# Kernel tuning notes

Hardware: AMD Instinct MI355X
Metric: run time of the kernel (lower is better)

The kernel has to match this reference:

```python
import jax, jax.numpy as jnp
import numpy as np

N, K, CIN, HID, COUT, E, MH = 8192, 200, 512, 256, 40, 5, 64
KG = K // E
EPS = 1e-5


def setup_inputs() -> dict:
    key = jax.random.key(0)
    ks = jax.random.split(key, 20)
    inp = {
        "X": jax.random.normal(ks[0], (N, CIN), jnp.float32),
        "La": jax.random.uniform(ks[1], (K,), jnp.float32),
        "U": jax.random.normal(ks[2], (N, K), jnp.float32),
        # 5 EigenExperts, each mlp = Linear(1,64) -> ReLU -> Linear(64,64) -> ReLU -> Linear(64,1)
        "eW1": jax.random.normal(ks[3], (E, MH), jnp.float32) * 0.5,
        "eb1": jax.random.normal(ks[4], (E, MH), jnp.float32) * 0.1,
        "eW2": jax.random.normal(ks[5], (E, MH, MH), jnp.float32) * (1.0 / np.sqrt(MH)),
        "eb2": jax.random.normal(ks[6], (E, MH), jnp.float32) * 0.1,
        "eW3": jax.random.normal(ks[7], (E, MH), jnp.float32) * (1.0 / np.sqrt(MH)),
        "eb3": jax.random.normal(ks[8], (E,), jnp.float32) * 0.1,
        # gate: Linear(5,5) -> ReLU -> Linear(5,5) -> Softmax
        "gW1": jax.random.normal(ks[9], (E, E), jnp.float32) * 0.4,
        "gb1": jax.random.normal(ks[10], (E,), jnp.float32) * 0.1,
        "gW2": jax.random.normal(ks[11], (E, E), jnp.float32) * 0.4,
        "gb2": jax.random.normal(ks[12], (E,), jnp.float32) * 0.1,
        # W: Linear(in_channels, hidden_dim)
        "Ww": jax.random.normal(ks[13], (CIN, HID), jnp.float32) * (1.0 / np.sqrt(CIN)),
        "Wb": jax.random.normal(ks[14], (HID,), jnp.float32) * 0.1,
        # BatchNorm1d(hidden_dim), training-mode batch stats
        "bn_gamma": jnp.ones((HID,), jnp.float32),
        "bn_beta": jnp.zeros((HID,), jnp.float32),
        # MLP: Linear(hidden_dim, out_channels)
        "Mw": jax.random.normal(ks[15], (HID, COUT), jnp.float32) * (1.0 / np.sqrt(HID)),
        "Mb": jax.random.normal(ks[16], (COUT,), jnp.float32) * 0.1,
    }
    return inp


def reference(X, La, U, eW1, eb1, eW2, eb2, eW3, eb3, gW1, gb1, gW2, gb2, Ww, Wb, bn_gamma, bn_beta, Mw, Mb):
    n, k = U.shape
    e = eW1.shape[0]
    kg = k // e
    # group eigenvector columns: U[:, i*kg:(i+1)*kg] for expert i -> [n, e, kg]
    Ue = U.reshape(n, e, kg)
    # EigenExpert tiny MLP applied elementwise over entries of each column, then mean over nodes
    h1 = jax.nn.relu(jnp.einsum('nek,eh->nekh', Ue, eW1) + eb1[None, :, None, :])
    h2 = jax.nn.relu(jnp.einsum('nekh,ehg->nekg', h1, eW2) + eb2[None, :, None, :])
    v = jnp.einsum('nekh,eh->nek', h2, eW3) + eb3[None, :, None]
    V = v.mean(axis=0)                      # [e, kg] importance per eigenvector
    # gate on per-group mean eigenvalue
    stats = La.reshape(e, kg).mean(axis=1)  # [e]
    g = jax.nn.relu(stats @ gW1 + gb1) @ gW2 + gb2
    g = jax.nn.softmax(g, axis=-1)          # [e]
    # sum_i g_i * U_i diag(V_i) U_i^T == (U * s) @ U^T with per-column scale s
    s = (g[:, None] * V).reshape(k)         # [k]
    A = (U * s[None, :]) @ U.T              # [n, n]
    out = A @ X                             # [n, cin]
    hidden = out @ Ww + Wb                  # [n, hid]
    mu = hidden.mean(axis=0)
    var = hidden.var(axis=0)                # biased, as torch BN uses for normalization
    h = (hidden - mu) * jax.lax.rsqrt(var + EPS) * bn_gamma + bn_beta
    h = jax.nn.relu(h)                      # dropout is identity (eval)
    logits = h @ Mw + Mb
    return jax.nn.log_softmax(logits, axis=1), hidden
```

## Files before the change

### kernel.cpp

```cpp
#include <hip/hip_runtime.h>
#include <hip/hip_bf16.h>

#define N_    8192
#define K_    200
#define CIN_  512
#define HID_  256
#define COUT_ 40
#define E_    5
#define MH_   64
#define KG_   40
#define EPS_  1e-5f

#define WS_VSUM  0
#define WS_BNSUM 256
#define WS_T     768
#define WS_S     103168
#define WS_G     103424

typedef __bf16 bf16x8 __attribute__((ext_vector_type(8)));
typedef _Float16 f16x2 __attribute__((ext_vector_type(2)));
typedef _Float16 f16x8 __attribute__((ext_vector_type(8)));
typedef float  f32x16 __attribute__((ext_vector_type(16)));

__device__ __forceinline__ uint packbf(float a, float b) {
    union { __bf16 h[2]; uint u; } p;
    p.h[0] = (__bf16)a; p.h[1] = (__bf16)b;
    return p.u;
}

union UB { uint4 q; bf16x8 v; };
union UHF { f16x2 h2[4]; f16x8 v; };

__global__ __launch_bounds__(256) void k_expert(
    const float* __restrict__ U,
    const float* __restrict__ eW1, const float* __restrict__ eb1,
    const float* __restrict__ eW2, const float* __restrict__ eb2,
    const float* __restrict__ eW3, const float* __restrict__ eb3,
    float* __restrict__ Vsum)
{
    const int e   = blockIdx.x;
    const int tid = threadIdx.x;
    const int w   = tid >> 6;
    const int l   = tid & 63;
    const int lo  = l & 31;
    const int hi  = l >> 5;

    __shared__ f16x2 sW1h[32], sb1h[32];
    __shared__ float sb2s[MH_], sW3s[MH_];
    __shared__ float colsum[4][48];

    if (tid < 32) {
        f16x2 w2; w2.x = (_Float16)eW1[e*MH_ + 2*tid]; w2.y = (_Float16)eW1[e*MH_ + 2*tid + 1];
        sW1h[tid] = w2;
        f16x2 b2; b2.x = (_Float16)eb1[e*MH_ + 2*tid]; b2.y = (_Float16)eb1[e*MH_ + 2*tid + 1];
        sb1h[tid] = b2;
    }
    if (tid < MH_) {
        sb2s[tid] = eb2[e*MH_ + tid];
        sW3s[tid] = eW3[e*MH_ + tid];
    }
    if (tid < 192) colsum[tid / 48][tid % 48] = 0.f;
    const float b3 = eb3[e];

    UHF fa[2][4];
    {
        const float* W2e = eW2 + e*MH_*MH_;
        #pragma unroll
        for (int mt = 0; mt < 2; ++mt) {
            const int grow = mt*32 + lo;
            #pragma unroll
            for (int t = 0; t < 4; ++t) {
                const int k0 = 16*t + 8*hi;
                #pragma unroll
                for (int r = 0; r < 4; ++r) {
                    f16x2 p;
                    p.x = (_Float16)W2e[(k0+2*r  )*MH_ + grow];
                    p.y = (_Float16)W2e[(k0+2*r+1)*MH_ + grow];
                    fa[mt][t].h2[r] = p;
                }
            }
        }
    }
    __syncthreads();

    f32x16 ci0, ci1;
    #pragma unroll
    for (int r = 0; r < 16; ++r) {
        const int gb = (r & 3) + 8*(r >> 2) + 4*hi;
        ci0[r] = sb2s[gb];
        ci1[r] = sb2s[32 + gb];
    }

    float uu[4]; int kgs[4];
    const int tile0 = blockIdx.y*16 + w*4;
    #pragma unroll
    for (int it = 0; it < 4; ++it) {
        const int idx = (tile0 + it)*32 + lo;
        const int n   = idx / KG_;
        const int kg  = idx - n*KG_;
        uu[it]  = U[n*K_ + e*KG_ + kg];
        kgs[it] = kg;
    }

    const f16x2 z2 = {(_Float16)0.f, (_Float16)0.f};

    #pragma unroll
    for (int it = 0; it < 4; ++it) {
        f16x2 u2; u2.x = (_Float16)uu[it]; u2.y = u2.x;

        f32x16 a0, a1;
        #pragma unroll
        for (int t = 0; t < 4; ++t) {
            const int kp = 8*t + 4*hi;
            UHF b;
            #pragma unroll
            for (int r = 0; r < 4; ++r)
                b.h2[r] = __builtin_elementwise_max(u2*sW1h[kp + r] + sb1h[kp + r], z2);
            if (t == 0) {
                a0 = __builtin_amdgcn_mfma_f32_32x32x16_f16(fa[0][0].v, b.v, ci0, 0, 0, 0);
                a1 = __builtin_amdgcn_mfma_f32_32x32x16_f16(fa[1][0].v, b.v, ci1, 0, 0, 0);
            } else {
                a0 = __builtin_amdgcn_mfma_f32_32x32x16_f16(fa[0][t].v, b.v, a0, 0, 0, 0);
                a1 = __builtin_amdgcn_mfma_f32_32x32x16_f16(fa[1][t].v, b.v, a1, 0, 0, 0);
            }
        }

        float p0 = 0.f, p1 = 0.f, p2 = 0.f, p3 = 0.f;
        #pragma unroll
        for (int r = 0; r < 16; r += 2) {
            const int g0 = (r & 3) + 8*(r >> 2) + 4*hi;
            const int g1 = ((r+1) & 3) + 8*((r+1) >> 2) + 4*hi;
            p0 += fmaxf(a0[r],   0.f) * sW3s[g0];
            p1 += fmaxf(a1[r],   0.f) * sW3s[32 + g0];
            p2 += fmaxf(a0[r+1], 0.f) * sW3s[g1];
            p3 += fmaxf(a1[r+1], 0.f) * sW3s[32 + g1];
        }
        float vs = (p0 + p1) + (p2 + p3);
        vs += __shfl_xor(vs, 32);
        if (hi == 0) atomicAdd(&colsum[w][kgs[it]], vs + b3);
    }

    __syncthreads();
    if (tid < KG_)
        atomicAdd(&Vsum[e*KG_ + tid],
                  colsum[0][tid] + colsum[1][tid] + colsum[2][tid] + colsum[3][tid]);
}

__global__ void k_gate(
    const float* __restrict__ La,
    const float* __restrict__ gW1, const float* __restrict__ gb1,
    const float* __restrict__ gW2, const float* __restrict__ gb2,
    const float* __restrict__ Vsum, float* __restrict__ s)
{
    __shared__ float sg[E_];
    const int tid = threadIdx.x;
    if (tid == 0) {
        float stats[E_], g1[E_], g2[E_];
        for (int e = 0; e < E_; ++e) {
            float acc = 0.f;
            for (int k = 0; k < KG_; ++k) acc += La[e*KG_ + k];
            stats[e] = acc * (1.0f/KG_);
        }
        for (int j = 0; j < E_; ++j) {
            float acc = gb1[j];
            for (int i = 0; i < E_; ++i) acc += stats[i]*gW1[i*E_ + j];
            g1[j] = fmaxf(acc, 0.f);
        }
        float m = -1e30f;
        for (int j = 0; j < E_; ++j) {
            float acc = gb2[j];
            for (int i = 0; i < E_; ++i) acc += g1[i]*gW2[i*E_ + j];
            g2[j] = acc;
            m = fmaxf(m, acc);
        }
        float ssum = 0.f;
        for (int j = 0; j < E_; ++j) { g2[j] = expf(g2[j]-m); ssum += g2[j]; }
        for (int j = 0; j < E_; ++j) sg[j] = g2[j] / ssum;
    }
    __syncthreads();
    if (tid < K_) s[tid] = sg[tid / KG_] * Vsum[tid] * (1.0f/N_);
}

__global__ __launch_bounds__(256) void k_utx(
    const float* __restrict__ U, const float* __restrict__ X,
    float* __restrict__ P)
{
    const int nc0 = blockIdx.x * 64;
    const int mc0 = blockIdx.y * 64;
    const int ks  = blockIdx.z;
    const int r0  = ks * 512;
    const int tid = threadIdx.x;
    const int w   = tid >> 6, l = tid & 63, lo = l & 31, hi = l >> 5;
    const int mq  = w >> 1, nq = w & 1;

    __shared__ uint sU[2][32][68];
    __shared__ uint sX[2][32][68];

    const int rpA = tid >> 4;
    const int rpB = rpA + 16;
    const int c4  = tid & 15;
    const int mcA = mc0 + 4*c4;
    const int xcA = nc0 + 4*c4;
    const int UMAX = N_*K_ - 4;

    float4 uA0,uA1,uB0,uB1,xA0,xA1,xB0,xB1;

#define UTX_LD(chunk) {                                                       \
    const int rb_ = r0 + 64*(chunk);                                          \
    uA0 = *reinterpret_cast<const float4*>(&U[min((rb_+2*rpA  )*K_ + mcA, UMAX)]); \
    uA1 = *reinterpret_cast<const float4*>(&U[min((rb_+2*rpA+1)*K_ + mcA, UMAX)]); \
    uB0 = *reinterpret_cast<const float4*>(&U[min((rb_+2*rpB  )*K_ + mcA, UMAX)]); \
    uB1 = *reinterpret_cast<const float4*>(&U[min((rb_+2*rpB+1)*K_ + mcA, UMAX)]); \
    xA0 = *reinterpret_cast<const float4*>(&X[(rb_+2*rpA  )*CIN_ + xcA]);     \
    xA1 = *reinterpret_cast<const float4*>(&X[(rb_+2*rpA+1)*CIN_ + xcA]);     \
    xB0 = *reinterpret_cast<const float4*>(&X[(rb_+2*rpB  )*CIN_ + xcA]);     \
    xB1 = *reinterpret_cast<const float4*>(&X[(rb_+2*rpB+1)*CIN_ + xcA]); }

#define UTX_WR(buf) {                                                         \
    uint4 p_;                                                                 \
    p_.x = packbf(uA0.x,uA1.x); p_.y = packbf(uA0.y,uA1.y);                   \
    p_.z = packbf(uA0.z,uA1.z); p_.w = packbf(uA0.w,uA1.w);                   \
    *reinterpret_cast<uint4*>(&sU[buf][rpA][4*c4]) = p_;                      \
    p_.x = packbf(uB0.x,uB1.x); p_.y = packbf(uB0.y,uB1.y);                   \
    p_.z = packbf(uB0.z,uB1.z); p_.w = packbf(uB0.w,uB1.w);                   \
    *reinterpret_cast<uint4*>(&sU[buf][rpB][4*c4]) = p_;                      \
    p_.x = packbf(xA0.x,xA1.x); p_.y = packbf(xA0.y,xA1.y);                   \
    p_.z = packbf(xA0.z,xA1.z); p_.w = packbf(xA0.w,xA1.w);                   \
    *reinterpret_cast<uint4*>(&sX[buf][rpA][4*c4]) = p_;                      \
    p_.x = packbf(xB0.x,xB1.x); p_.y = packbf(xB0.y,xB1.y);                   \
    p_.z = packbf(xB0.z,xB1.z); p_.w = packbf(xB0.w,xB1.w);                   \
    *reinterpret_cast<uint4*>(&sX[buf][rpB][4*c4]) = p_; }

#define UTX_MM(buf) {                                                         \
    _Pragma("unroll") for (int ksi = 0; ksi < 4; ++ksi) {                     \
        const int rp0_ = 8*ksi + 4*hi;                                        \
        UB a_, b_;                                                            \
        a_.q.x = sU[buf][rp0_+0][32*mq+lo];                                   \
        a_.q.y = sU[buf][rp0_+1][32*mq+lo];                                   \
        a_.q.z = sU[buf][rp0_+2][32*mq+lo];                                   \
        a_.q.w = sU[buf][rp0_+3][32*mq+lo];                                   \
        b_.q.x = sX[buf][rp0_+0][32*nq+lo];                                   \
        b_.q.y = sX[buf][rp0_+1][32*nq+lo];                                   \
        b_.q.z = sX[buf][rp0_+2][32*nq+lo];                                   \
        b_.q.w = sX[buf][rp0_+3][32*nq+lo];                                   \
        acc = __builtin_amdgcn_mfma_f32_32x32x16_bf16(a_.v, b_.v, acc, 0,0,0); } }

    f32x16 acc = {0};
    UTX_LD(0);
    UTX_WR(0);
    __syncthreads();
    #pragma unroll
    for (int t = 0; t < 8; ++t) {
        if (t < 7) UTX_LD(t+1);
        UTX_MM(t & 1);
        if (t < 7) UTX_WR((t+1) & 1);
        __syncthreads();
    }

    #pragma unroll
    for (int r = 0; r < 16; ++r) {
        const int mrow = mc0 + mq*32 + (r & 3) + 8*(r >> 2) + 4*hi;
        const int ncol = nc0 + nq*32 + lo;
        P[(ks*256 + mrow)*512 + ncol] = acc[r];
    }
#undef UTX_LD
#undef UTX_WR
#undef UTX_MM
}

__global__ __launch_bounds__(256) void k_red(
    const float* __restrict__ P, float* __restrict__ T)
{
    const int j  = blockIdx.x*256 + threadIdx.x;
    const int m  = j >> 7;
    const int c4 = j & 127;
    float4 s4 = {0.f, 0.f, 0.f, 0.f};
    for (int ks = 0; ks < 16; ++ks) {
        const float4 v = *reinterpret_cast<const float4*>(&P[(ks*256 + m)*512 + 4*c4]);
        s4.x += v.x; s4.y += v.y; s4.z += v.z; s4.w += v.w;
    }
    *reinterpret_cast<float4*>(&T[m*512 + 4*c4]) = s4;
}

__global__ __launch_bounds__(256) void k_g(
    const float* __restrict__ T, const float* __restrict__ Ww,
    float* __restrict__ G)
{
    const int k0  = blockIdx.x * 4;
    const int c   = threadIdx.x;
    __shared__ float4 sT4[4][128];

    for (int j = threadIdx.x; j < 512; j += 256) {
        const int r = j >> 7, c4 = j & 127;
        sT4[r][c4] = reinterpret_cast<const float4*>(T)[(k0+r)*128 + c4];
    }
    __syncthreads();

    float a0 = 0.f, a1 = 0.f, a2 = 0.f, a3 = 0.f;
    for (int ci4 = 0; ci4 < 128; ++ci4) {
        const float w0 = Ww[(4*ci4+0)*HID_ + c];
        const float w1 = Ww[(4*ci4+1)*HID_ + c];
        const float w2 = Ww[(4*ci4+2)*HID_ + c];
        const float w3 = Ww[(4*ci4+3)*HID_ + c];
        float4 t;
        t = sT4[0][ci4]; a0 += t.x*w0 + t.y*w1 + t.z*w2 + t.w*w3;
        t = sT4[1][ci4]; a1 += t.x*w0 + t.y*w1 + t.z*w2 + t.w*w3;
        t = sT4[2][ci4]; a2 += t.x*w0 + t.y*w1 + t.z*w2 + t.w*w3;
        t = sT4[3][ci4]; a3 += t.x*w0 + t.y*w1 + t.z*w2 + t.w*w3;
    }
    G[(k0+0)*HID_ + c] = a0;
    G[(k0+1)*HID_ + c] = a1;
    G[(k0+2)*HID_ + c] = a2;
    G[(k0+3)*HID_ + c] = a3;
}

__global__ __launch_bounds__(256) void k_hidden(
    const float* __restrict__ U, const float* __restrict__ s,
    const float* __restrict__ G, const float* __restrict__ Wb,
    float* __restrict__ hid, float* __restrict__ bnsum)
{
    const int c0  = blockIdx.x * 32;
    const int n0  = blockIdx.y * 128;
    const int tid = threadIdx.x;
    const int w   = tid >> 6;
    const int l   = tid & 63;
    const int lo  = l & 31;
    const int hi  = l >> 5;

    __shared__ uint  sA[104][129];
    __shared__ uint  sB[104][33];
    __shared__ float ss[208];

    if (tid < 208) ss[tid] = (tid < K_) ? s[tid] : 0.f;
    __syncthreads();

    #pragma unroll
    for (int u = 0; u < 13; ++u) {
        const int j  = tid + u*256;
        const int m  = j & 127, kq = j >> 7;
        float4 a = {0,0,0,0}, b = {0,0,0,0};
        if (kq < 25) {
            a = *reinterpret_cast<const float4*>(&U[(n0+m)*K_ + 8*kq]);
            b = *reinterpret_cast<const float4*>(&U[(n0+m)*K_ + 8*kq + 4]);
            a.x *= ss[8*kq+0]; a.y *= ss[8*kq+1]; a.z *= ss[8*kq+2]; a.w *= ss[8*kq+3];
            b.x *= ss[8*kq+4]; b.y *= ss[8*kq+5]; b.z *= ss[8*kq+6]; b.w *= ss[8*kq+7];
        }
        sA[4*kq+0][m] = packbf(a.x, a.y);
        sA[4*kq+1][m] = packbf(a.z, a.w);
        sA[4*kq+2][m] = packbf(b.x, b.y);
        sA[4*kq+3][m] = packbf(b.z, b.w);
    }
    for (int j = tid; j < 832; j += 256) {
        const int c = j & 31, kq = j >> 5;
        float g[8];
        #pragma unroll
        for (int i = 0; i < 8; ++i)
            g[i] = (kq < 25) ? G[(8*kq+i)*HID_ + c0 + c] : 0.f;
        sB[4*kq+0][c] = packbf(g[0], g[1]);
        sB[4*kq+1][c] = packbf(g[2], g[3]);
        sB[4*kq+2][c] = packbf(g[4], g[5]);
        sB[4*kq+3][c] = packbf(g[6], g[7]);
    }
    __syncthreads();

    f32x16 acc = {0};
    #pragma unroll
    for (int t = 0; t < 13; ++t) {
        const int rp0 = 8*t + 4*hi;
        UB a_, b_;
        a_.q.x = sA[rp0+0][32*w + lo];
        a_.q.y = sA[rp0+1][32*w + lo];
        a_.q.z = sA[rp0+2][32*w + lo];
        a_.q.w = sA[rp0+3][32*w + lo];
        b_.q.x = sB[rp0+0][lo];
        b_.q.y = sB[rp0+1][lo];
        b_.q.z = sB[rp0+2][lo];
        b_.q.w = sB[rp0+3][lo];
        acc = __builtin_amdgcn_mfma_f32_32x32x16_bf16(a_.v, b_.v, acc, 0, 0, 0);
    }

    const float wb = Wb[c0 + lo];
    float sm = 0.f, sq = 0.f;
    #pragma unroll
    for (int r = 0; r < 16; ++r) {
        const int row = 32*w + (r & 3) + 8*(r >> 2) + 4*hi;
        const float h = acc[r] + wb;
        hid[(n0+row)*HID_ + c0 + lo] = h;
        sm += h; sq += h*h;
    }
    sm += __shfl_xor(sm, 32); sq += __shfl_xor(sq, 32);
    if (hi == 0) {
        atomicAdd(&bnsum[c0 + lo],        sm);
        atomicAdd(&bnsum[HID_ + c0 + lo], sq);
    }
}

__global__ __launch_bounds__(256) void k_logits(
    const float* __restrict__ hid, const float* __restrict__ bnsum,
    const float* __restrict__ gamma, const float* __restrict__ beta,
    const float* __restrict__ Mw, const float* __restrict__ Mb,
    float* __restrict__ outls)
{
    __shared__ float sc[HID_], sh[HID_], sMb[COUT_];
    __shared__ float sMw[HID_][COUT_];
    __shared__ float sPart[8][32][41];

    const int tid = threadIdx.x;
    const int r   = tid & 31;
    const int sl  = tid >> 5;

    {
        const float sm = bnsum[tid], sq = bnsum[HID_+tid];
        const float mu  = sm * (1.0f/N_);
        const float var = sq * (1.0f/N_) - mu*mu;
        const float a   = gamma[tid] * rsqrtf(var + EPS_);
        sc[tid] = a;
        sh[tid] = beta[tid] - mu*a;
    }
    for (int j = tid; j < HID_*COUT_/4; j += 256)
        reinterpret_cast<float4*>(&sMw[0][0])[j] = reinterpret_cast<const float4*>(Mw)[j];
    if (tid < COUT_) sMb[tid] = Mb[tid];
    __syncthreads();

    const int n  = blockIdx.x*32 + r;
    const int cb = sl * 32;
    float acc[COUT_];
    #pragma unroll
    for (int j = 0; j < COUT_; ++j) acc[j] = 0.f;

    const float4* hrow = reinterpret_cast<const float4*>(&hid[n*HID_ + cb]);
    #pragma unroll
    for (int c4 = 0; c4 < 8; ++c4) {
        const float4 h4 = hrow[c4];
        const float hv[4] = {h4.x, h4.y, h4.z, h4.w};
        #pragma unroll
        for (int q = 0; q < 4; ++q) {
            const int c = cb + 4*c4 + q;
            const float hn = fmaxf(hv[q]*sc[c] + sh[c], 0.f);
            #pragma unroll
            for (int j0 = 0; j0 < COUT_; j0 += 4) {
                const float4 wv = *reinterpret_cast<const float4*>(&sMw[c][j0]);
                acc[j0+0] += hn*wv.x; acc[j0+1] += hn*wv.y;
                acc[j0+2] += hn*wv.z; acc[j0+3] += hn*wv.w;
            }
        }
    }
    #pragma unroll
    for (int j = 0; j < COUT_; ++j) sPart[sl][r][j] = acc[j];
    __syncthreads();

    if (tid < 32) {
        const int n2 = blockIdx.x*32 + tid;
        float a2[COUT_];
        #pragma unroll
        for (int j = 0; j < COUT_; ++j) {
            float sum = sMb[j];
            #pragma unroll
            for (int s2 = 0; s2 < 8; ++s2) sum += sPart[s2][tid][j];
            a2[j] = sum;
        }
        float m = -1e30f;
        #pragma unroll
        for (int j = 0; j < COUT_; ++j) m = fmaxf(m, a2[j]);
        float ssum = 0.f;
        #pragma unroll
        for (int j = 0; j < COUT_; ++j) ssum += expf(a2[j] - m);
        const float lse = m + logf(ssum);
        #pragma unroll
        for (int j = 0; j < COUT_; ++j)
            outls[n2*COUT_ + j] = a2[j] - lse;
    }
}

extern "C" void kernel_launch(void* const* d_in, const int* in_sizes, int n_in,
                              void* d_out, int out_size, void* d_ws, size_t ws_size,
                              hipStream_t stream)
{
    const float* X        = (const float*)d_in[0];
    const float* La       = (const float*)d_in[1];
    const float* U        = (const float*)d_in[2];
    const float* eW1      = (const float*)d_in[3];
    const float* eb1      = (const float*)d_in[4];
    const float* eW2      = (const float*)d_in[5];
    const float* eb2      = (const float*)d_in[6];
    const float* eW3      = (const float*)d_in[7];
    const float* eb3      = (const float*)d_in[8];
    const float* gW1      = (const float*)d_in[9];
    const float* gb1      = (const float*)d_in[10];
    const float* gW2      = (const float*)d_in[11];
    const float* gb2      = (const float*)d_in[12];
    const float* Ww       = (const float*)d_in[13];
    const float* Wb       = (const float*)d_in[14];
    const float* bn_gamma = (const float*)d_in[15];
    const float* bn_beta  = (const float*)d_in[16];
    const float* Mw       = (const float*)d_in[17];
    const float* Mb       = (const float*)d_in[18];

    float* out   = (float*)d_out;
    float* ws    = (float*)d_ws;
    float* Vsum  = ws + WS_VSUM;
    float* bnsum = ws + WS_BNSUM;
    float* T     = ws + WS_T;
    float* s     = ws + WS_S;
    float* G     = ws + WS_G;

    float* outls = out;
    float* hid   = out + N_*COUT_;
    float* P     = out;

    (void)hipMemsetAsync(ws, 0, (size_t)768 * sizeof(float), stream);

    k_utx   <<<dim3(8, 4, 16), 256, 0, stream>>>(U, X, P);
    k_expert<<<dim3(E_, 640),  256, 0, stream>>>(U, eW1, eb1, eW2, eb2, eW3, eb3, Vsum);
    k_gate  <<<1,   256, 0, stream>>>(La, gW1, gb1, gW2, gb2, Vsum, s);
    k_red   <<<100, 256, 0, stream>>>(P, T);
    k_g     <<<50,  256, 0, stream>>>(T, Ww, G);
    k_hidden<<<dim3(8, 64), 256, 0, stream>>>(U, s, G, Wb, hid, bnsum);
    k_logits<<<256, 256, 0, stream>>>(hid, bnsum, bn_gamma, bn_beta, Mw, Mb, outls);
}
```

Baseline: 210.7 us.

## Merge U^T X and expert kernels into one launch; fuse reduce, gate and G

```diff
diff --git a/kernel.cpp b/kernel.cpp
--- a/kernel.cpp
+++ b/kernel.cpp
@@ -13,7 +13,6 @@
 
 #define WS_VSUM  0
 #define WS_BNSUM 256
-#define WS_T     768
 #define WS_S     103168
 #define WS_G     103424
 
@@ -31,179 +30,41 @@
 union UB { uint4 q; bf16x8 v; };
 union UHF { f16x2 h2[4]; f16x8 v; };
 
-__global__ __launch_bounds__(256) void k_expert(
-    const float* __restrict__ U,
+__global__ __launch_bounds__(256) void k_fused1(
+    const float* __restrict__ U, const float* __restrict__ X,
+    float* __restrict__ P,
     const float* __restrict__ eW1, const float* __restrict__ eb1,
     const float* __restrict__ eW2, const float* __restrict__ eb2,
     const float* __restrict__ eW3, const float* __restrict__ eb3,
     float* __restrict__ Vsum)
 {
-    const int e   = blockIdx.x;
+    __shared__ __align__(16) char ldsraw[34816];
     const int tid = threadIdx.x;
     const int w   = tid >> 6;
     const int l   = tid & 63;
     const int lo  = l & 31;
     const int hi  = l >> 5;
 
-    __shared__ f16x2 sW1h[32], sb1h[32];
-    __shared__ float sb2s[MH_], sW3s[MH_];
-    __shared__ float colsum[4][48];
-
-    if (tid < 32) {
-        f16x2 w2; w2.x = (_Float16)eW1[e*MH_ + 2*tid]; w2.y = (_Float16)eW1[e*MH_ + 2*tid + 1];
-        sW1h[tid] = w2;
-        f16x2 b2; b2.x = (_Float16)eb1[e*MH_ + 2*tid]; b2.y = (_Float16)eb1[e*MH_ + 2*tid + 1];
-        sb1h[tid] = b2;
-    }
-    if (tid < MH_) {
-        sb2s[tid] = eb2[e*MH_ + tid];
-        sW3s[tid] = eW3[e*MH_ + tid];
-    }
-    if (tid < 192) colsum[tid / 48][tid % 48] = 0.f;
-    const float b3 = eb3[e];
-
-    UHF fa[2][4];
-    {
-        const float* W2e = eW2 + e*MH_*MH_;
-        #pragma unroll
-        for (int mt = 0; mt < 2; ++mt) {
-            const int grow = mt*32 + lo;
-            #pragma unroll
-            for (int t = 0; t < 4; ++t) {
-                const int k0 = 16*t + 8*hi;
-                #pragma unroll
-                for (int r = 0; r < 4; ++r) {
-                    f16x2 p;
-                    p.x = (_Float16)W2e[(k0+2*r  )*MH_ + grow];
-                    p.y = (_Float16)W2e[(k0+2*r+1)*MH_ + grow];
-                    fa[mt][t].h2[r] = p;
-                }
-            }
-        }
-    }
-    __syncthreads();
-
-    f32x16 ci0, ci1;
-    #pragma unroll
-    for (int r = 0; r < 16; ++r) {
-        const int gb = (r & 3) + 8*(r >> 2) + 4*hi;
-        ci0[r] = sb2s[gb];
-        ci1[r] = sb2s[32 + gb];
-    }
-
-    float uu[4]; int kgs[4];
-    const int tile0 = blockIdx.y*16 + w*4;
-    #pragma unroll
-    for (int it = 0; it < 4; ++it) {
-        const int idx = (tile0 + it)*32 + lo;
-        const int n   = idx / KG_;
-        const int kg  = idx - n*KG_;
-        uu[it]  = U[n*K_ + e*KG_ + kg];
-        kgs[it] = kg;
-    }
-
-    const f16x2 z2 = {(_Float16)0.f, (_Float16)0.f};
-
-    #pragma unroll
-    for (int it = 0; it < 4; ++it) {
-        f16x2 u2; u2.x = (_Float16)uu[it]; u2.y = u2.x;
-
-        f32x16 a0, a1;
-        #pragma unroll
-        for (int t = 0; t < 4; ++t) {
-            const int kp = 8*t + 4*hi;
-            UHF b;
-            #pragma unroll
-            for (int r = 0; r < 4; ++r)
-                b.h2[r] = __builtin_elementwise_max(u2*sW1h[kp + r] + sb1h[kp + r], z2);
-            if (t == 0) {
-                a0 = __builtin_amdgcn_mfma_f32_32x32x16_f16(fa[0][0].v, b.v, ci0, 0, 0, 0);
-                a1 = __builtin_amdgcn_mfma_f32_32x32x16_f16(fa[1][0].v, b.v, ci1, 0, 0, 0);
-            } else {
-                a0 = __builtin_amdgcn_mfma_f32_32x32x16_f16(fa[0][t].v, b.v, a0, 0, 0, 0);
-                a1 = __builtin_amdgcn_mfma_f32_32x32x16_f16(fa[1][t].v, b.v, a1, 0, 0, 0);
-            }
-        }
-
-        float p0 = 0.f, p1 = 0.f, p2 = 0.f, p3 = 0.f;
-        #pragma unroll
-        for (int r = 0; r < 16; r += 2) {
-            const int g0 = (r & 3) + 8*(r >> 2) + 4*hi;
-            const int g1 = ((r+1) & 3) + 8*((r+1) >> 2) + 4*hi;
-            p0 += fmaxf(a0[r],   0.f) * sW3s[g0];
-            p1 += fmaxf(a1[r],   0.f) * sW3s[32 + g0];
-            p2 += fmaxf(a0[r+1], 0.f) * sW3s[g1];
-            p3 += fmaxf(a1[r+1], 0.f) * sW3s[32 + g1];
-        }
-        float vs = (p0 + p1) + (p2 + p3);
-        vs += __shfl_xor(vs, 32);
-        if (hi == 0) atomicAdd(&colsum[w][kgs[it]], vs + b3);
-    }
-
-    __syncthreads();
-    if (tid < KG_)
-        atomicAdd(&Vsum[e*KG_ + tid],
-                  colsum[0][tid] + colsum[1][tid] + colsum[2][tid] + colsum[3][tid]);
-}
-
-__global__ void k_gate(
-    const float* __restrict__ La,
-    const float* __restrict__ gW1, const float* __restrict__ gb1,
-    const float* __restrict__ gW2, const float* __restrict__ gb2,
-    const float* __restrict__ Vsum, float* __restrict__ s)
-{
-    __shared__ float sg[E_];
-    const int tid = threadIdx.x;
-    if (tid == 0) {
-        float stats[E_], g1[E_], g2[E_];
-        for (int e = 0; e < E_; ++e) {
-            float acc = 0.f;
-            for (int k = 0; k < KG_; ++k) acc += La[e*KG_ + k];
-            stats[e] = acc * (1.0f/KG_);
-        }
-        for (int j = 0; j < E_; ++j) {
-            float acc = gb1[j];
-            for (int i = 0; i < E_; ++i) acc += stats[i]*gW1[i*E_ + j];
-            g1[j] = fmaxf(acc, 0.f);
-        }
-        float m = -1e30f;
-        for (int j = 0; j < E_; ++j) {
-            float acc = gb2[j];
-            for (int i = 0; i < E_; ++i) acc += g1[i]*gW2[i*E_ + j];
-            g2[j] = acc;
-            m = fmaxf(m, acc);
-        }
-        float ssum = 0.f;
-        for (int j = 0; j < E_; ++j) { g2[j] = expf(g2[j]-m); ssum += g2[j]; }
-        for (int j = 0; j < E_; ++j) sg[j] = g2[j] / ssum;
-    }
-    __syncthreads();
-    if (tid < K_) s[tid] = sg[tid / KG_] * Vsum[tid] * (1.0f/N_);
-}
-
-__global__ __launch_bounds__(256) void k_utx(
-    const float* __restrict__ U, const float* __restrict__ X,
-    float* __restrict__ P)
-{
-    const int nc0 = blockIdx.x * 64;
-    const int mc0 = blockIdx.y * 64;
-    const int ks  = blockIdx.z;
-    const int r0  = ks * 512;
-    const int tid = threadIdx.x;
-    const int w   = tid >> 6, l = tid & 63, lo = l & 31, hi = l >> 5;
-    const int mq  = w >> 1, nq = w & 1;
-
-    __shared__ uint sU[2][32][68];
-    __shared__ uint sX[2][32][68];
-
-    const int rpA = tid >> 4;
-    const int rpB = rpA + 16;
-    const int c4  = tid & 15;
-    const int mcA = mc0 + 4*c4;
-    const int xcA = nc0 + 4*c4;
-    const int UMAX = N_*K_ - 4;
-
-    float4 uA0,uA1,uB0,uB1,xA0,xA1,xB0,xB1;
+    if (blockIdx.x < 512) {
+        const int bid = blockIdx.x;
+        const int nc0 = (bid & 7) * 64;
+        const int mc0 = ((bid >> 3) & 3) * 64;
+        const int ks  = bid >> 5;
+        const int r0  = ks * 512;
+        const int mq  = w >> 1, nq = w & 1;
+
+        typedef uint UtxBuf[32][68];
+        UtxBuf* sU = reinterpret_cast<UtxBuf*>(ldsraw);
+        UtxBuf* sX = reinterpret_cast<UtxBuf*>(ldsraw + 17408);
+
+        const int rpA = tid >> 4;
+        const int rpB = rpA + 16;
+        const int c4  = tid & 15;
+        const int mcA = mc0 + 4*c4;
+        const int xcA = nc0 + 4*c4;
+        const int UMAX = N_*K_ - 4;
+
+        float4 uA0,uA1,uB0,uB1,xA0,xA1,xB0,xB1;
 
 #define UTX_LD(chunk) {                                                       \
     const int rb_ = r0 + 64*(chunk);                                          \
@@ -245,57 +106,195 @@
         b_.q.w = sX[buf][rp0_+3][32*nq+lo];                                   \
         acc = __builtin_amdgcn_mfma_f32_32x32x16_bf16(a_.v, b_.v, acc, 0,0,0); } }
 
-    f32x16 acc = {0};
-    UTX_LD(0);
-    UTX_WR(0);
-    __syncthreads();
-    #pragma unroll
-    for (int t = 0; t < 8; ++t) {
-        if (t < 7) UTX_LD(t+1);
-        UTX_MM(t & 1);
-        if (t < 7) UTX_WR((t+1) & 1);
+        f32x16 acc = {0};
+        UTX_LD(0);
+        UTX_WR(0);
         __syncthreads();
-    }
-
-    #pragma unroll
-    for (int r = 0; r < 16; ++r) {
-        const int mrow = mc0 + mq*32 + (r & 3) + 8*(r >> 2) + 4*hi;
-        const int ncol = nc0 + nq*32 + lo;
-        P[(ks*256 + mrow)*512 + ncol] = acc[r];
-    }
+        #pragma unroll
+        for (int t = 0; t < 8; ++t) {
+            if (t < 7) UTX_LD(t+1);
+            UTX_MM(t & 1);
+            if (t < 7) UTX_WR((t+1) & 1);
+            __syncthreads();
+        }
+
+        #pragma unroll
+        for (int r = 0; r < 16; ++r) {
+            const int mrow = mc0 + mq*32 + (r & 3) + 8*(r >> 2) + 4*hi;
+            const int ncol = nc0 + nq*32 + lo;
+            P[(ks*256 + mrow)*512 + ncol] = acc[r];
+        }
 #undef UTX_LD
 #undef UTX_WR
 #undef UTX_MM
+        return;
+    }
+
+    {
+        const int t5 = blockIdx.x - 512;
+        const int e  = t5 % E_;
+        const int by = t5 / E_;
+
+        struct ExLds {
+            f16x2 sW1h[32]; f16x2 sb1h[32];
+            float sb2s[MH_]; float sW3s[MH_];
+            float colsum[4][48];
+        };
+        ExLds& S = *reinterpret_cast<ExLds*>(ldsraw);
+
+        if (tid < 32) {
+            f16x2 w2; w2.x = (_Float16)eW1[e*MH_ + 2*tid]; w2.y = (_Float16)eW1[e*MH_ + 2*tid + 1];
+            S.sW1h[tid] = w2;
+            f16x2 b2; b2.x = (_Float16)eb1[e*MH_ + 2*tid]; b2.y = (_Float16)eb1[e*MH_ + 2*tid + 1];
+            S.sb1h[tid] = b2;
+        }
+        if (tid < MH_) {
+            S.sb2s[tid] = eb2[e*MH_ + tid];
+            S.sW3s[tid] = eW3[e*MH_ + tid];
+        }
+        if (tid < 192) S.colsum[tid / 48][tid % 48] = 0.f;
+        const float b3 = eb3[e];
+
+        UHF fa[2][4];
+        {
+            const float* W2e = eW2 + e*MH_*MH_;
+            #pragma unroll
+            for (int mt = 0; mt < 2; ++mt) {
+                const int grow = mt*32 + lo;
+                #pragma unroll
+                for (int t = 0; t < 4; ++t) {
+                    const int k0 = 16*t + 8*hi;
+                    #pragma unroll
+                    for (int r = 0; r < 4; ++r) {
+                        f16x2 p;
+                        p.x = (_Float16)W2e[(k0+2*r  )*MH_ + grow];
+                        p.y = (_Float16)W2e[(k0+2*r+1)*MH_ + grow];
+                        fa[mt][t].h2[r] = p;
+                    }
+                }
+            }
+        }
+        __syncthreads();
+
+        f32x16 ci0, ci1;
+        #pragma unroll
+        for (int r = 0; r < 16; ++r) {
+            const int gb = (r & 3) + 8*(r >> 2) + 4*hi;
+            ci0[r] = S.sb2s[gb];
+            ci1[r] = S.sb2s[32 + gb];
+        }
+
+        float uu[4]; int kgs[4];
+        const int tile0 = by*16 + w*4;
+        #pragma unroll
+        for (int it = 0; it < 4; ++it) {
+            const int idx = (tile0 + it)*32 + lo;
+            const int n   = idx / KG_;
+            const int kg  = idx - n*KG_;
+            uu[it]  = U[n*K_ + e*KG_ + kg];
+            kgs[it] = kg;
+        }
+
+        const f16x2 z2 = {(_Float16)0.f, (_Float16)0.f};
+
+        #pragma unroll
+        for (int it = 0; it < 4; ++it) {
+            f16x2 u2; u2.x = (_Float16)uu[it]; u2.y = u2.x;
+
+            f32x16 a0, a1;
+            #pragma unroll
+            for (int t = 0; t < 4; ++t) {
+                const int kp = 8*t + 4*hi;
+                UHF b;
+                #pragma unroll
+                for (int r = 0; r < 4; ++r)
+                    b.h2[r] = __builtin_elementwise_max(u2*S.sW1h[kp + r] + S.sb1h[kp + r], z2);
+                if (t == 0) {
+                    a0 = __builtin_amdgcn_mfma_f32_32x32x16_f16(fa[0][0].v, b.v, ci0, 0, 0, 0);
+                    a1 = __builtin_amdgcn_mfma_f32_32x32x16_f16(fa[1][0].v, b.v, ci1, 0, 0, 0);
+                } else {
+                    a0 = __builtin_amdgcn_mfma_f32_32x32x16_f16(fa[0][t].v, b.v, a0, 0, 0, 0);
+                    a1 = __builtin_amdgcn_mfma_f32_32x32x16_f16(fa[1][t].v, b.v, a1, 0, 0, 0);
+                }
+            }
+
+            float p0 = 0.f, p1 = 0.f, p2 = 0.f, p3 = 0.f;
+            #pragma unroll
+            for (int r = 0; r < 16; r += 2) {
+                const int g0 = (r & 3) + 8*(r >> 2) + 4*hi;
+                const int g1 = ((r+1) & 3) + 8*((r+1) >> 2) + 4*hi;
+                p0 += fmaxf(a0[r],   0.f) * S.sW3s[g0];
+                p1 += fmaxf(a1[r],   0.f) * S.sW3s[32 + g0];
+                p2 += fmaxf(a0[r+1], 0.f) * S.sW3s[g1];
+                p3 += fmaxf(a1[r+1], 0.f) * S.sW3s[32 + g1];
+            }
+            float vs = (p0 + p1) + (p2 + p3);
+            vs += __shfl_xor(vs, 32);
+            if (hi == 0) atomicAdd(&S.colsum[w][kgs[it]], vs + b3);
+        }
+
+        __syncthreads();
+        if (tid < KG_)
+            atomicAdd(&Vsum[e*KG_ + tid],
+                      S.colsum[0][tid] + S.colsum[1][tid] + S.colsum[2][tid] + S.colsum[3][tid]);
+    }
 }
 
-__global__ __launch_bounds__(256) void k_red(
-    const float* __restrict__ P, float* __restrict__ T)
+__global__ __launch_bounds__(256) void k_rgg(
+    const float* __restrict__ P, const float* __restrict__ Ww,
+    const float* __restrict__ La,
+    const float* __restrict__ gW1, const float* __restrict__ gb1,
+    const float* __restrict__ gW2, const float* __restrict__ gb2,
+    const float* __restrict__ Vsum,
+    float* __restrict__ s, float* __restrict__ G)
 {
-    const int j  = blockIdx.x*256 + threadIdx.x;
-    const int m  = j >> 7;
-    const int c4 = j & 127;
-    float4 s4 = {0.f, 0.f, 0.f, 0.f};
-    for (int ks = 0; ks < 16; ++ks) {
-        const float4 v = *reinterpret_cast<const float4*>(&P[(ks*256 + m)*512 + 4*c4]);
-        s4.x += v.x; s4.y += v.y; s4.z += v.z; s4.w += v.w;
-    }
-    *reinterpret_cast<float4*>(&T[m*512 + 4*c4]) = s4;
-}
-
-__global__ __launch_bounds__(256) void k_g(
-    const float* __restrict__ T, const float* __restrict__ Ww,
-    float* __restrict__ G)
-{
-    const int k0  = blockIdx.x * 4;
-    const int c   = threadIdx.x;
+    const int tid = threadIdx.x;
+
+    if (blockIdx.x == 50) {
+        __shared__ float sg[E_];
+        if (tid == 0) {
+            float stats[E_], g1[E_], g2[E_];
+            for (int e = 0; e < E_; ++e) {
+                float acc = 0.f;
+                for (int k = 0; k < KG_; ++k) acc += La[e*KG_ + k];
+                stats[e] = acc * (1.0f/KG_);
+            }
+            for (int j = 0; j < E_; ++j) {
+                float acc = gb1[j];
+                for (int i = 0; i < E_; ++i) acc += stats[i]*gW1[i*E_ + j];
+                g1[j] = fmaxf(acc, 0.f);
+            }
+            float m = -1e30f;
+            for (int j = 0; j < E_; ++j) {
+                float acc = gb2[j];
+                for (int i = 0; i < E_; ++i) acc += g1[i]*gW2[i*E_ + j];
+                g2[j] = acc;
+                m = fmaxf(m, acc);
+            }
+            float ssum = 0.f;
+            for (int j = 0; j < E_; ++j) { g2[j] = expf(g2[j]-m); ssum += g2[j]; }
+            for (int j = 0; j < E_; ++j) sg[j] = g2[j] / ssum;
+        }
+        __syncthreads();
+        if (tid < K_) s[tid] = sg[tid / KG_] * Vsum[tid] * (1.0f/N_);
+        return;
+    }
+
     __shared__ float4 sT4[4][128];
-
-    for (int j = threadIdx.x; j < 512; j += 256) {
+    const int k0 = blockIdx.x * 4;
+
+    for (int j = tid; j < 512; j += 256) {
         const int r = j >> 7, c4 = j & 127;
-        sT4[r][c4] = reinterpret_cast<const float4*>(T)[(k0+r)*128 + c4];
+        float4 a = {0.f, 0.f, 0.f, 0.f};
+        for (int ks = 0; ks < 16; ++ks) {
+            const float4 v = *reinterpret_cast<const float4*>(&P[(ks*256 + k0 + r)*512 + 4*c4]);
+            a.x += v.x; a.y += v.y; a.z += v.z; a.w += v.w;
+        }
+        sT4[r][c4] = a;
     }
     __syncthreads();
 
+    const int c = tid;
     float a0 = 0.f, a1 = 0.f, a2 = 0.f, a3 = 0.f;
     for (int ci4 = 0; ci4 < 128; ++ci4) {
         const float w0 = Ww[(4*ci4+0)*HID_ + c];
@@ -500,7 +499,6 @@
     float* ws    = (float*)d_ws;
     float* Vsum  = ws + WS_VSUM;
     float* bnsum = ws + WS_BNSUM;
-    float* T     = ws + WS_T;
     float* s     = ws + WS_S;
     float* G     = ws + WS_G;
 
@@ -510,11 +508,8 @@
 
     (void)hipMemsetAsync(ws, 0, (size_t)768 * sizeof(float), stream);
 
-    k_utx   <<<dim3(8, 4, 16), 256, 0, stream>>>(U, X, P);
-    k_expert<<<dim3(E_, 640),  256, 0, stream>>>(U, eW1, eb1, eW2, eb2, eW3, eb3, Vsum);
-    k_gate  <<<1,   256, 0, stream>>>(La, gW1, gb1, gW2, gb2, Vsum, s);
-    k_red   <<<100, 256, 0, stream>>>(P, T);
-    k_g     <<<50,  256, 0, stream>>>(T, Ww, G);
+    k_fused1<<<3712, 256, 0, stream>>>(U, X, P, eW1, eb1, eW2, eb2, eW3, eb3, Vsum);
+    k_rgg   <<<51,   256, 0, stream>>>(P, Ww, La, gW1, gb1, gW2, gb2, Vsum, s, G);
     k_hidden<<<dim3(8, 64), 256, 0, stream>>>(U, s, G, Wb, hid, bnsum);
-    k_logits<<<256, 256, 0, stream>>>(hid, bnsum, bn_gamma, bn_beta, Mw, Mb, outls);
+    k_logits<<<256,  256, 0, stream>>>(hid, bnsum, bn_gamma, bn_beta, Mw, Mb, outls);
 }
```

Result: faster. 201.3 us (-4.4%).
